# Optimization experiments

Measured on AMD Instinct MI355X. Metric: run time of the kernel, lower is better.

## Reference

```python
import jax, jax.numpy as jnp
import numpy as np

ALPHA = 0.2  # leaky relu slope
NEG = -1e9


def setup_inputs() -> dict:
    key = jax.random.key(0)
    ks = jax.random.split(key, 8)
    B, N, F_IN, H, HID, OUT = 2, 4096, 512, 4, 128, 64
    x = jax.random.normal(ks[0], (B, N, F_IN), dtype=jnp.float32)
    adj = jax.random.randint(ks[1], (B, N, N), 0, 2, dtype=jnp.int32)
    s_in = float(np.sqrt(2.0 / (F_IN + HID)))
    W_heads = jax.random.normal(ks[2], (H, HID, F_IN), dtype=jnp.float32) * s_in
    a1_heads = jax.random.normal(ks[3], (H, HID), dtype=jnp.float32) * 0.1
    a2_heads = jax.random.normal(ks[4], (H, HID), dtype=jnp.float32) * 0.1
    s_out = float(np.sqrt(2.0 / (H * HID + OUT)))
    W_out = jax.random.normal(ks[5], (OUT, H * HID), dtype=jnp.float32) * s_out
    a1_out = jax.random.normal(ks[6], (OUT,), dtype=jnp.float32) * 0.1
    a2_out = jax.random.normal(ks[7], (OUT,), dtype=jnp.float32) * 0.1
    return {"x": x, "adj": adj, "W_heads": W_heads, "a1_heads": a1_heads,
            "a2_heads": a2_heads, "W_out": W_out, "a1_out": a1_out, "a2_out": a2_out}


def _gat_layer(x, adj, W, a1, a2, concat):
    # x: [B,N,F], W: [O,F], a1/a2: [O]
    h = jnp.einsum('bnf,of->bno', x, W)            # [B,N,O]
    f1 = jnp.einsum('bno,o->bn', h, a1)            # [B,N]
    f2 = jnp.einsum('bno,o->bn', h, a2)            # [B,N]
    e = f1[:, :, None] + f2[:, None, :]            # [B,N,N] additive scores
    e = jnp.where(e > 0, e, ALPHA * e)             # leaky relu
    e = jnp.where(adj == 0, NEG, e)                # adjacency mask
    att = jax.nn.softmax(e, axis=2)
    h_prime = jnp.einsum('bnm,bmo->bno', att, h)
    return jax.nn.elu(h_prime) if concat else h_prime


def reference(x, adj, W_heads, a1_heads, a2_heads, W_out, a1_out, a2_out):
    H = W_heads.shape[0]
    heads = [_gat_layer(x, adj, W_heads[i], a1_heads[i], a2_heads[i], True)
             for i in range(H)]
    x_cat = jnp.concatenate(heads, axis=2)         # [B,N,H*HID]
    return _gat_layer(x_cat, adj, W_out, a1_out, a2_out, False)
```

## Files before the change

kernel.cpp:

```cpp
#include <hip/hip_runtime.h>

#define TB 2
#define TN 4096
#define TH 4
#define THID 128
#define TOUT 64
#define NW 128

using f4    = __attribute__((ext_vector_type(4))) float;
using s16x8 = __attribute__((ext_vector_type(8))) short;
using s16x4 = __attribute__((ext_vector_type(4))) short;
using u32x4 = __attribute__((ext_vector_type(4))) unsigned;

static __device__ __forceinline__ short f2bf(float f){
  unsigned u = __float_as_uint(f);
  unsigned r = u + 0x7FFFu + ((u >> 16) & 1u);
  return (short)(r >> 16);
}
static __device__ __forceinline__ float bf2f(short s){
  return __uint_as_float(((unsigned)(unsigned short)s) << 16);
}
static __device__ __forceinline__ unsigned encf(float f){
  unsigned u = __float_as_uint(f);
  return (u & 0x80000000u) ? ~u : (u | 0x80000000u);
}
static __device__ __forceinline__ float decf(unsigned u){
  unsigned v = (u & 0x80000000u) ? (u & 0x7FFFFFFFu) : ~u;
  return __uint_as_float(v);
}
static __device__ __forceinline__ void gll16(const void* g, void* l){
  __builtin_amdgcn_global_load_lds((const __attribute__((address_space(1))) unsigned int*)g,
                                   (__attribute__((address_space(3))) unsigned int*)l, 16, 0, 0);
}
static __device__ __forceinline__ f4 mfma_bf16(s16x8 a, s16x8 b, f4 c){
  return __builtin_amdgcn_mfma_f32_16x16x32_bf16(a, b, c, 0, 0, 0);
}

__global__ void k_pack(const int* __restrict__ adj, unsigned* __restrict__ adjT,
                       unsigned* __restrict__ mx){
  if (blockIdx.x == 0 && threadIdx.x < 16) mx[threadIdx.x] = 0;
  int t = blockIdx.x * 256 + threadIdx.x;
  int n = t & 4095, w = (t >> 12) & 127, b = t >> 19;
  const int4* p = (const int4*)(adj + ((size_t)(b*TN + n))*TN + w*32);
  unsigned m = 0;
#pragma unroll
  for (int i = 0; i < 8; ++i){
    int4 v = p[i];
    m |= (v.x != 0 ? 1u : 0u) << (i*4+0);
    m |= (v.y != 0 ? 1u : 0u) << (i*4+1);
    m |= (v.z != 0 ? 1u : 0u) << (i*4+2);
    m |= (v.w != 0 ? 1u : 0u) << (i*4+3);
  }
  adjT[((size_t)(b*NW + w))*TN + n] = m;
}

__global__ void k_split(const float* __restrict__ x, short* __restrict__ hi, short* __restrict__ lo){
  int t = blockIdx.x * 256 + threadIdx.x;
  f4 v = ((const f4*)x)[t];
  s16x4 h, l;
#pragma unroll
  for (int e = 0; e < 4; ++e){
    short hb = f2bf(v[e]);
    h[e] = hb;
    l[e] = f2bf(v[e] - bf2f(hb));
  }
  ((s16x4*)hi)[t] = h;
  ((s16x4*)lo)[t] = l;
}
__global__ void k_cvt(const float* __restrict__ x, short* __restrict__ o){
  int t = blockIdx.x * 256 + threadIdx.x;
  f4 v = ((const f4*)x)[t];
  s16x4 h;
#pragma unroll
  for (int e = 0; e < 4; ++e) h[e] = f2bf(v[e]);
  ((s16x4*)o)[t] = h;
}

__global__ __launch_bounds__(512, 2) void k_gemm1(
    const short* __restrict__ xh, const short* __restrict__ xl,
    const short* __restrict__ wh, const short* __restrict__ wl,
    const float* __restrict__ a1h, const float* __restrict__ a2h,
    short* __restrict__ hTb, float* __restrict__ f1g,
    float* __restrict__ Qa, float* __restrict__ Sa, unsigned* __restrict__ mx){
  __shared__ short tiles[2][4][8192];
  __shared__ float red[2][128][2];
  __shared__ float bmx[2];
  int tid = threadIdx.x, lane = tid & 63, w = tid >> 6;
  int kgrp = lane >> 4, li = lane & 15;
  int nblk = blockIdx.x >> 6, mblk = blockIdx.x & 63;
  int n0 = nblk * 128, m0 = mblk * 128;
  int wn = w >> 2, wm = w & 3;
  const f4 fz = {0.f, 0.f, 0.f, 0.f};
  f4 acc[4][2];
#pragma unroll
  for (int i = 0; i < 4; ++i)
#pragma unroll
    for (int j = 0; j < 2; ++j) acc[i][j] = fz;

#pragma unroll
  for (int tno = 0; tno < 4; ++tno){
    const short* gb = (tno==0 ? wh : tno==1 ? wl : tno==2 ? xh : xl);
    int r0 = (tno < 2) ? n0 : m0;
#pragma unroll
    for (int i = 0; i < 2; ++i){
      int s = (i*8 + w)*64 + lane;
      int row = s >> 3, c = s & 7, cs = c ^ (row & 7);
      gll16(gb + (size_t)(r0 + row)*512 + cs*8, (char*)tiles[0][tno] + (i*8+w)*1024);
    }
  }
  asm volatile("s_waitcnt vmcnt(0)" ::: "memory");
  __syncthreads();

  for (int kt = 0; kt < 8; ++kt){
    int cur = kt & 1;
    if (kt < 7){
      int k0 = (kt+1) * 64;
#pragma unroll
      for (int tno = 0; tno < 4; ++tno){
        const short* gb = (tno==0 ? wh : tno==1 ? wl : tno==2 ? xh : xl);
        int r0 = (tno < 2) ? n0 : m0;
#pragma unroll
        for (int i = 0; i < 2; ++i){
          int s = (i*8 + w)*64 + lane;
          int row = s >> 3, c = s & 7, cs = c ^ (row & 7);
          gll16(gb + (size_t)(r0 + row)*512 + k0 + cs*8, (char*)tiles[cur^1][tno] + (i*8+w)*1024);
        }
      }
    }
    const char* t0 = (const char*)tiles[cur][0];
    const char* t1 = (const char*)tiles[cur][1];
    const char* t2 = (const char*)tiles[cur][2];
    const char* t3 = (const char*)tiles[cur][3];
#pragma unroll
    for (int ks = 0; ks < 2; ++ks){
      int ck = ks*4 + kgrp;
      s16x8 ah[4], al[4], bh[2], bl[2];
#pragma unroll
      for (int fn = 0; fn < 4; ++fn){
        int row = wn*64 + fn*16 + li;
        int off = row*128 + ((ck ^ (row & 7)) << 4);
        ah[fn] = *(const s16x8*)(t0 + off);
        al[fn] = *(const s16x8*)(t1 + off);
      }
#pragma unroll
      for (int fm = 0; fm < 2; ++fm){
        int row = wm*32 + fm*16 + li;
        int off = row*128 + ((ck ^ (row & 7)) << 4);
        bh[fm] = *(const s16x8*)(t2 + off);
        bl[fm] = *(const s16x8*)(t3 + off);
      }
#pragma unroll
      for (int fn = 0; fn < 4; ++fn)
#pragma unroll
        for (int fm = 0; fm < 2; ++fm)
          acc[fn][fm] = mfma_bf16(ah[fn], bh[fm], acc[fn][fm]);
#pragma unroll
      for (int fn = 0; fn < 4; ++fn)
#pragma unroll
        for (int fm = 0; fm < 2; ++fm)
          acc[fn][fm] = mfma_bf16(ah[fn], bl[fm], acc[fn][fm]);
#pragma unroll
      for (int fn = 0; fn < 4; ++fn)
#pragma unroll
        for (int fm = 0; fm < 2; ++fm)
          acc[fn][fm] = mfma_bf16(al[fn], bh[fm], acc[fn][fm]);
    }
    asm volatile("s_waitcnt vmcnt(0)" ::: "memory");
    __syncthreads();
  }
  int head = nblk;
#pragma unroll
  for (int fn = 0; fn < 4; ++fn){
#pragma unroll
    for (int fm = 0; fm < 2; ++fm){
#pragma unroll
      for (int r = 0; r < 4; ++r){
        int nout = n0 + wn*64 + fn*16 + kgrp*4 + r;
        int m = m0 + wm*32 + fm*16 + li;
        int b = m >> 12, n = m & 4095;
        int hid = nout & 127;
        size_t idx = ((size_t)((b*TH + head)*THID + hid))*TN + n;
        hTb[idx] = f2bf(acc[fn][fm][r]);
      }
    }
  }
  const float* a1p = a1h + head*THID;
  const float* a2p = a2h + head*THID;
  float s1[2] = {0.f, 0.f}, s2[2] = {0.f, 0.f};
#pragma unroll
  for (int fn = 0; fn < 4; ++fn)
#pragma unroll
    for (int r = 0; r < 4; ++r){
      int row = wn*64 + fn*16 + kgrp*4 + r;
      float w1 = a1p[row], w2 = a2p[row];
#pragma unroll
      for (int fm = 0; fm < 2; ++fm){
        s1[fm] = fmaf(acc[fn][fm][r], w1, s1[fm]);
        s2[fm] = fmaf(acc[fn][fm][r], w2, s2[fm]);
      }
    }
#pragma unroll
  for (int fm = 0; fm < 2; ++fm){
    s1[fm] += __shfl_xor(s1[fm], 16); s1[fm] += __shfl_xor(s1[fm], 32);
    s2[fm] += __shfl_xor(s2[fm], 16); s2[fm] += __shfl_xor(s2[fm], 32);
  }
  if (kgrp == 0){
#pragma unroll
    for (int fm = 0; fm < 2; ++fm){
      int col = wm*32 + fm*16 + li;
      red[wn][col][0] = s1[fm];
      red[wn][col][1] = s2[fm];
    }
  }
  __syncthreads();
  if (tid < 128){
    float f1v = red[0][tid][0] + red[1][tid][0];
    float f2v = red[0][tid][1] + red[1][tid][1];
    int m = m0 + tid, b = m >> 12, n = m & 4095;
    int idx = (b*TH + head)*TN + n;
    f1g[idx] = f1v;
    Qa[idx] = expf(f2v);
    Sa[idx] = expf(0.2f*f2v);
    float wmx = f2v;
#pragma unroll
    for (int d = 1; d < 64; d <<= 1) wmx = fmaxf(wmx, __shfl_xor(wmx, d));
    if ((tid & 63) == 0) bmx[tid >> 6] = wmx;
  }
  __syncthreads();
  if (tid == 0){
    int b = m0 >> 12;
    atomicMax(&mx[b*TH + head], encf(fmaxf(bmx[0], bmx[1])));
  }
}

__global__ __launch_bounds__(256, 2) void k_attn1(
    const short* __restrict__ hTb, const float* __restrict__ f1,
    const float* __restrict__ Qa, const float* __restrict__ Sa,
    const unsigned* __restrict__ adjT, const unsigned* __restrict__ mx,
    short* __restrict__ part, float* __restrict__ sums){
  __shared__ short tile[4][8192];
  __shared__ float Qs[1024], Ss[1024];
  __shared__ unsigned abuf[4][256];
  int tid = threadIdx.x, lane = tid & 63, w = tid >> 6;
  int kgrp = lane >> 4, li = lane & 15;
  int bid = blockIdx.x;
  int js = bid >> 8, b = (bid >> 7) & 1, h = (bid >> 5) & 3, rblk = bid & 31;
  int bh = b*TH + h;
  int jbase = js * 1024;
  int r0b = rblk * 128;
  const short* hbase = hTb + ((size_t)bh*THID)*TN;
  const float* Qrow = Qa + (size_t)bh*TN + jbase;
  const float* Srow = Sa + (size_t)bh*TN + jbase;

  auto STAGE = [&](int t){
    int jg = jbase + t*64;
    char* dst = (char*)tile[t & 3];
#pragma unroll
    for (int i = 0; i < 4; ++i){
      int s = (i*4 + w)*64 + lane;
      int row = s >> 3, c = s & 7, cs = c ^ (row & 7);
      gll16(hbase + (size_t)row*TN + jg + cs*8, dst + (i*4+w)*1024);
    }
    int w0 = jg >> 5;
    gll16(adjT + (size_t)(b*NW + w0 + (lane>>5))*TN + r0b + (lane&31)*4, (char*)abuf[t & 3]);
  };

  gll16(Qrow + w*256 + lane*4, (char*)Qs + w*1024);
  gll16(Srow + w*256 + lane*4, (char*)Ss + w*1024);
  STAGE(0); STAGE(1); STAGE(2);

  int r0 = r0b + w*32;
  float Pv[2], Rv[2];
  int lrow[2];
  float mf = decf(mx[bh]);
#pragma unroll
  for (int rf = 0; rf < 2; ++rf){
    int row = r0 + rf*16 + li;
    lrow[rf] = w*32 + rf*16 + li;
    float f1v = f1[bh*TN + row];
    float e = f1v + mf;
    float m = e > 0.f ? e : 0.2f*e;
    Pv[rf] = expf(f1v - m);
    Rv[rf] = expf(0.2f*f1v - m);
  }
  const f4 fz = {0.f,0.f,0.f,0.f};
  f4 acc[2][8];
#pragma unroll
  for (int i = 0; i < 2; ++i)
#pragma unroll
    for (int j = 0; j < 8; ++j) acc[i][j] = fz;
  f4 accs[2] = {fz, fz};
  s16x8 ones;
#pragma unroll
  for (int e = 0; e < 8; ++e) ones[e] = (short)0x3F80;

  for (int jt = 0; jt < 16; ++jt){
    if (jt < 14)       asm volatile("s_waitcnt vmcnt(10)" ::: "memory");
    else if (jt == 14) asm volatile("s_waitcnt vmcnt(5)" ::: "memory");
    else               asm volatile("s_waitcnt vmcnt(0)" ::: "memory");
    __builtin_amdgcn_s_barrier();
    __builtin_amdgcn_sched_barrier(0);
    if (jt < 13) STAGE(jt + 3);

    int j0 = jt*64;
    const char* tp = (const char*)tile[jt & 3];
    const unsigned* ab = abuf[jt & 3];
    unsigned aw0[2], aw1[2];
#pragma unroll
    for (int rf = 0; rf < 2; ++rf){
      aw0[rf] = ab[lrow[rf]];
      aw1[rf] = ab[128 + lrow[rf]];
    }
#pragma unroll
    for (int ks = 0; ks < 2; ++ks){
      int jloc = j0 + ks*32 + kgrp*8;
      float qv[8], sv[8];
      *(f4*)&qv[0] = *(const f4*)&Qs[jloc];
      *(f4*)&qv[4] = *(const f4*)&Qs[jloc+4];
      *(f4*)&sv[0] = *(const f4*)&Ss[jloc];
      *(f4*)&sv[4] = *(const f4*)&Ss[jloc+4];
      s16x8 af[2];
#pragma unroll
      for (int rf = 0; rf < 2; ++rf){
        unsigned word = ks ? aw1[rf] : aw0[rf];
        unsigned byt = (word >> (kgrp*8)) & 0xFFu;
        float P = Pv[rf], R = Rv[rf];
        u32x4 pw;
#pragma unroll
        for (int pe = 0; pe < 4; ++pe){
          float va = fmaxf(P*qv[2*pe],   R*sv[2*pe]);
          float vb = fmaxf(P*qv[2*pe+1], R*sv[2*pe+1]);
          va = (byt & (1u << (2*pe)))   ? va : 0.f;
          vb = (byt & (1u << (2*pe+1))) ? vb : 0.f;
          unsigned ua = __float_as_uint(va) + 0x8000u;
          unsigned ub = __float_as_uint(vb) + 0x8000u;
          pw[pe] = __builtin_amdgcn_perm(ub, ua, 0x07060302);
        }
        af[rf] = __builtin_bit_cast(s16x8, pw);
      }
      accs[0] = mfma_bf16(af[0], ones, accs[0]);
      accs[1] = mfma_bf16(af[1], ones, accs[1]);
#pragma unroll
      for (int cf = 0; cf < 8; ++cf){
        int col = cf*16 + li;
        int off = col*128 + (((ks*4 + kgrp) ^ (col & 7)) << 4);
        s16x8 bfr = *(const s16x8*)(tp + off);
        acc[0][cf] = mfma_bf16(af[0], bfr, acc[0][cf]);
        acc[1][cf] = mfma_bf16(af[1], bfr, acc[1][cf]);
      }
    }
  }
  int sl = js*8 + bh;
  if (li == 0){
#pragma unroll
    for (int rf = 0; rf < 2; ++rf)
#pragma unroll
      for (int r = 0; r < 4; ++r)
        sums[(size_t)sl*TN + r0 + rf*16 + kgrp*4 + r] = accs[rf][r];
  }
#pragma unroll
  for (int rf = 0; rf < 2; ++rf)
#pragma unroll
    for (int cf = 0; cf < 8; ++cf)
#pragma unroll
      for (int r = 0; r < 4; ++r){
        int row = r0 + rf*16 + kgrp*4 + r;
        int hid = cf*16 + li;
        part[((size_t)sl*TN + row)*THID + hid] = f2bf(acc[rf][cf][r]);
      }
}

__global__ void k_comb1(const short* __restrict__ part, const float* __restrict__ sums,
                        short* __restrict__ xcat){
  int t = blockIdx.x*256 + threadIdx.x;
  int hid8 = t & 15, n = (t >> 4) & 4095, h = (t >> 16) & 3, b = t >> 18;
  int bh = b*TH + h;
  float a[8] = {0,0,0,0,0,0,0,0};
  float s = 0.f;
#pragma unroll
  for (int js = 0; js < 4; ++js){
    size_t rowoff = (size_t)(js*8 + bh)*TN + n;
    s16x8 pv = *(const s16x8*)(part + rowoff*THID + hid8*8);
#pragma unroll
    for (int e = 0; e < 8; ++e) a[e] += bf2f(pv[e]);
    s += sums[rowoff];
  }
  float inv = 1.f / s;
  s16x8 o;
#pragma unroll
  for (int e = 0; e < 8; ++e){
    float x = a[e] * inv;
    o[e] = f2bf(x > 0.f ? x : expm1f(x));
  }
  *(s16x8*)(xcat + ((size_t)(b*TN + n))*512 + h*128 + hid8*8) = o;
}

__global__ __launch_bounds__(128) void k_gemm2(
    const short* __restrict__ xcat, const short* __restrict__ wo,
    const float* __restrict__ a1o, const float* __restrict__ a2o,
    short* __restrict__ h2T, float* __restrict__ f1o,
    float* __restrict__ Q2, float* __restrict__ S2, unsigned* __restrict__ mx2){
  int tid = threadIdx.x, lane = tid & 63, w = tid >> 6;
  int kgrp = lane >> 4, li = lane & 15;
  int m0 = blockIdx.x * 32;
  const f4 fz = {0.f,0.f,0.f,0.f};
  f4 acc[4] = {fz, fz, fz, fz};
  int rowA = m0 + w*16 + li;
  for (int kt = 0; kt < 16; ++kt){
    int k = kt*32 + kgrp*8;
    s16x8 a = *(const s16x8*)(xcat + (size_t)rowA*512 + k);
#pragma unroll
    for (int cf = 0; cf < 4; ++cf){
      int col = cf*16 + li;
      s16x8 bfr = *(const s16x8*)(wo + (size_t)col*512 + k);
      acc[cf] = mfma_bf16(a, bfr, acc[cf]);
    }
  }
  float p1[4] = {0,0,0,0}, p2[4] = {0,0,0,0};
#pragma unroll
  for (int cf = 0; cf < 4; ++cf){
    int o = cf*16 + li;
    float w1 = a1o[o], w2 = a2o[o];
#pragma unroll
    for (int r = 0; r < 4; ++r){
      p1[r] = fmaf(acc[cf][r], w1, p1[r]);
      p2[r] = fmaf(acc[cf][r], w2, p2[r]);
    }
  }
#pragma unroll
  for (int r = 0; r < 4; ++r){
#pragma unroll
    for (int d = 1; d < 16; d <<= 1){
      p1[r] += __shfl_xor(p1[r], d);
      p2[r] += __shfl_xor(p2[r], d);
    }
  }
#pragma unroll
  for (int cf = 0; cf < 4; ++cf)
#pragma unroll
    for (int r = 0; r < 4; ++r){
      int row = m0 + w*16 + kgrp*4 + r;
      int o = cf*16 + li;
      int b = row >> 12, n = row & 4095;
      h2T[((size_t)(b*TOUT + o))*TN + n] = f2bf(acc[cf][r]);
    }
  if (li == 0){
#pragma unroll
    for (int r = 0; r < 4; ++r){
      int row = m0 + w*16 + kgrp*4 + r;
      f1o[row] = p1[r];
      Q2[row] = expf(p2[r]);
      S2[row] = expf(0.2f*p2[r]);
    }
  }
  float m2 = fmaxf(fmaxf(p2[0], p2[1]), fmaxf(p2[2], p2[3]));
  m2 = fmaxf(m2, __shfl_xor(m2, 16));
  m2 = fmaxf(m2, __shfl_xor(m2, 32));
  __shared__ float bm[2];
  if (lane == 0) bm[w] = m2;
  __syncthreads();
  if (tid == 0) atomicMax(&mx2[m0 >> 12], encf(fmaxf(bm[0], bm[1])));
}

__global__ __launch_bounds__(256, 3) void k_attn2(
    const short* __restrict__ h2T, const float* __restrict__ f1o,
    const float* __restrict__ Q2, const float* __restrict__ S2,
    const unsigned* __restrict__ adjT, const unsigned* __restrict__ mx2,
    float* __restrict__ part, float* __restrict__ sums){
  __shared__ short tile[4][4096];
  __shared__ float Qs[1024], Ss[1024];
  __shared__ unsigned abuf[4][128];
  int tid = threadIdx.x, lane = tid & 63, w = tid >> 6;
  int kgrp = lane >> 4, li = lane & 15;
  int bid = blockIdx.x;
  int js = bid >> 7, b = (bid >> 6) & 1, rblk = bid & 63;
  int jbase = js * 1024;
  int r0b = rblk * 64;
  const short* hbase = h2T + (size_t)b*TOUT*TN;
  const float* Qrow = Q2 + (size_t)b*TN + jbase;
  const float* Srow = S2 + (size_t)b*TN + jbase;

  auto STAGE = [&](int t){
    int jg = jbase + t*64;
    char* dst = (char*)tile[t & 3];
#pragma unroll
    for (int i = 0; i < 2; ++i){
      int s = (i*4 + w)*64 + lane;
      int row = s >> 3, c = s & 7, cs = c ^ (row & 7);
      gll16(hbase + (size_t)row*TN + jg + cs*8, dst + (i*4+w)*1024);
    }
    int w0 = jg >> 5;
    if (lane < 32)
      gll16(adjT + (size_t)(b*NW + w0 + (lane>>4))*TN + r0b + (lane&15)*4, (char*)abuf[t & 3]);
  };

  gll16(Qrow + w*256 + lane*4, (char*)Qs + w*1024);
  gll16(Srow + w*256 + lane*4, (char*)Ss + w*1024);
  STAGE(0); STAGE(1); STAGE(2);

  int r0 = r0b + w*16;
  int lrow = w*16 + li;
  float mf = decf(mx2[b]);
  float f1v = f1o[b*TN + r0 + li];
  float e0 = f1v + mf;
  float m0v = e0 > 0.f ? e0 : 0.2f*e0;
  float Pv = expf(f1v - m0v);
  float Rv = expf(0.2f*f1v - m0v);
  const f4 fz = {0.f,0.f,0.f,0.f};
  f4 acc[4] = {fz, fz, fz, fz};
  f4 accs = fz;
  s16x8 ones;
#pragma unroll
  for (int e = 0; e < 8; ++e) ones[e] = (short)0x3F80;

  for (int jt = 0; jt < 16; ++jt){
    if (jt < 14)       asm volatile("s_waitcnt vmcnt(6)" ::: "memory");
    else if (jt == 14) asm volatile("s_waitcnt vmcnt(3)" ::: "memory");
    else               asm volatile("s_waitcnt vmcnt(0)" ::: "memory");
    __builtin_amdgcn_s_barrier();
    __builtin_amdgcn_sched_barrier(0);
    if (jt < 13) STAGE(jt + 3);

    int j0 = jt*64;
    const char* tp = (const char*)tile[jt & 3];
    const unsigned* ab = abuf[jt & 3];
    unsigned aw0 = ab[lrow], aw1 = ab[64 + lrow];
#pragma unroll
    for (int ks = 0; ks < 2; ++ks){
      int jloc = j0 + ks*32 + kgrp*8;
      float qv[8], sv[8];
      *(f4*)&qv[0] = *(const f4*)&Qs[jloc];
      *(f4*)&qv[4] = *(const f4*)&Qs[jloc+4];
      *(f4*)&sv[0] = *(const f4*)&Ss[jloc];
      *(f4*)&sv[4] = *(const f4*)&Ss[jloc+4];
      unsigned word = ks ? aw1 : aw0;
      unsigned byt = (word >> (kgrp*8)) & 0xFFu;
      u32x4 pw;
#pragma unroll
      for (int pe = 0; pe < 4; ++pe){
        float va = fmaxf(Pv*qv[2*pe],   Rv*sv[2*pe]);
        float vb = fmaxf(Pv*qv[2*pe+1], Rv*sv[2*pe+1]);
        va = (byt & (1u << (2*pe)))   ? va : 0.f;
        vb = (byt & (1u << (2*pe+1))) ? vb : 0.f;
        unsigned ua = __float_as_uint(va) + 0x8000u;
        unsigned ub = __float_as_uint(vb) + 0x8000u;
        pw[pe] = __builtin_amdgcn_perm(ub, ua, 0x07060302);
      }
      s16x8 af = __builtin_bit_cast(s16x8, pw);
      accs = mfma_bf16(af, ones, accs);
#pragma unroll
      for (int cf = 0; cf < 4; ++cf){
        int col = cf*16 + li;
        int off = col*128 + (((ks*4 + kgrp) ^ (col & 7)) << 4);
        s16x8 bfr = *(const s16x8*)(tp + off);
        acc[cf] = mfma_bf16(af, bfr, acc[cf]);
      }
    }
  }
  int sl = js*2 + b;
  if (li == 0){
#pragma unroll
    for (int r = 0; r < 4; ++r)
      sums[(size_t)sl*TN + r0 + kgrp*4 + r] = accs[r];
  }
#pragma unroll
  for (int cf = 0; cf < 4; ++cf)
#pragma unroll
    for (int r = 0; r < 4; ++r){
      int row = r0 + kgrp*4 + r;
      int o = cf*16 + li;
      part[((size_t)sl*TN + row)*TOUT + o] = acc[cf][r];
    }
}

__global__ void k_comb2(const float* __restrict__ part, const float* __restrict__ sums,
                        float* __restrict__ out){
  int t = blockIdx.x*256 + threadIdx.x;
  int o4 = t & 15, n = (t >> 4) & 4095, b = t >> 16;
  f4 a = {0.f,0.f,0.f,0.f};
  float s = 0.f;
#pragma unroll
  for (int js = 0; js < 4; ++js){
    int sl = js*2 + b;
    a += ((const f4*)part)[((size_t)sl*TN + n)*16 + o4];
    s += sums[(size_t)sl*TN + n];
  }
  f4 r = a / s;
  ((f4*)out)[((size_t)(b*TN + n))*16 + o4] = r;
}

extern "C" void kernel_launch(void* const* d_in, const int* in_sizes, int n_in,
                              void* d_out, int out_size, void* d_ws, size_t ws_size,
                              hipStream_t stream) {
  (void)in_sizes; (void)n_in; (void)out_size; (void)ws_size;
  const float* x       = (const float*)d_in[0];
  const int*   adj     = (const int*)d_in[1];
  const float* W_heads = (const float*)d_in[2];
  const float* a1h     = (const float*)d_in[3];
  const float* a2h     = (const float*)d_in[4];
  const float* W_out   = (const float*)d_in[5];
  const float* a1o     = (const float*)d_in[6];
  const float* a2o     = (const float*)d_in[7];

  char* p = (char*)d_ws;
  auto alloc = [&](size_t sz){ char* r = p; p += (sz + 255) & ~(size_t)255; return r; };
  unsigned* adjT  = (unsigned*) alloc(4ull*1048576);
  short*    wo    = (short*)    alloc(2ull*32768);
  short*    hTb   = (short*)    alloc(2ull*4194304);
  float*    f1    = (float*)    alloc(4ull*32768);
  float*    Qa    = (float*)    alloc(4ull*32768);
  float*    Sa    = (float*)    alloc(4ull*32768);
  unsigned* mx    = (unsigned*) alloc(4ull*16);
  short*    xcat  = (short*)    alloc(2ull*4194304);
  float*    f1o   = (float*)    alloc(4ull*8192);
  float*    Q2    = (float*)    alloc(4ull*8192);
  float*    S2    = (float*)    alloc(4ull*8192);
  short*    h2T   = (short*)    alloc(2ull*524288);
  float*    sums1 = (float*)    alloc(4ull*131072);
  float*    sums2 = (float*)    alloc(4ull*65536);
  char* A = alloc(33554432ull);
  short* xh   = (short*)A;
  short* xl   = (short*)(A + 8388608);
  short* part1 = (short*)A;
  char* Bu = alloc(16777216ull);
  short* wh = (short*)Bu;
  short* wl = (short*)(Bu + 524288);
  float* part2 = (float*)Bu;

  k_pack <<<4096, 256, 0, stream>>>(adj, adjT, mx);
  k_split<<<4096, 256, 0, stream>>>(x, xh, xl);
  k_split<<<256, 256, 0, stream>>>(W_heads, wh, wl);
  k_cvt  <<<32, 256, 0, stream>>>(W_out, wo);
  k_gemm1<<<256, 512, 0, stream>>>(xh, xl, wh, wl, a1h, a2h, hTb, f1, Qa, Sa, mx);
  k_attn1<<<1024, 256, 0, stream>>>(hTb, f1, Qa, Sa, adjT, mx, part1, sums1);
  k_comb1<<<2048, 256, 0, stream>>>(part1, sums1, xcat);
  k_gemm2<<<256, 128, 0, stream>>>(xcat, wo, a1o, a2o, h2T, f1o, Q2, S2, mx + 8);
  k_attn2<<<512, 256, 0, stream>>>(h2T, f1o, Q2, S2, adjT, mx + 8, part2, sums2);
  k_comb2<<<512, 256, 0, stream>>>(part2, sums2, (float*)d_out);
}
```

Baseline: 153.6 us.

## Enlarge attention row tiles and re-split key range with triple buffering

In k_attn1 each block now covers 256 rows (four 16-row fragments per wave) instead of 128, so each staged 64-key hidden tile is reused across twice as many rows and the grid is halved. In k_attn2 row tiles double to 128 and the key range is split into eight 512-wide slices instead of four, which keeps the grid size and doubles the partials that k_comb2 reduces. Both kernels move from 4-deep to 3-deep staging buffers and retune the waitcnt thresholds. The cost is far more accumulator registers in attn1 (4x8 fragments), which may cut occupancy, along with a shallower prefetch pipeline.

Measured after the change: 148.0 us. 3.7% less time.

```diff
diff --git a/kernel.cpp b/kernel.cpp
--- a/kernel.cpp
+++ b/kernel.cpp
@@ -238,23 +238,24 @@
     const float* __restrict__ Qa, const float* __restrict__ Sa,
     const unsigned* __restrict__ adjT, const unsigned* __restrict__ mx,
     short* __restrict__ part, float* __restrict__ sums){
-  __shared__ short tile[4][8192];
+  __shared__ short tile[3][8192];
   __shared__ float Qs[1024], Ss[1024];
-  __shared__ unsigned abuf[4][256];
+  __shared__ unsigned abuf[3][512];
   int tid = threadIdx.x, lane = tid & 63, w = tid >> 6;
   int kgrp = lane >> 4, li = lane & 15;
   int bid = blockIdx.x;
-  int js = bid >> 8, b = (bid >> 7) & 1, h = (bid >> 5) & 3, rblk = bid & 31;
+  int js = bid >> 7, b = (bid >> 6) & 1, h = (bid >> 4) & 3, rblk = bid & 15;
   int bh = b*TH + h;
   int jbase = js * 1024;
-  int r0b = rblk * 128;
+  int r0b = rblk * 256;
   const short* hbase = hTb + ((size_t)bh*THID)*TN;
   const float* Qrow = Qa + (size_t)bh*TN + jbase;
   const float* Srow = Sa + (size_t)bh*TN + jbase;
 
   auto STAGE = [&](int t){
     int jg = jbase + t*64;
-    char* dst = (char*)tile[t & 3];
+    int bi = t % 3;
+    char* dst = (char*)tile[bi];
 #pragma unroll
     for (int i = 0; i < 4; ++i){
       int s = (i*4 + w)*64 + lane;
@@ -262,21 +263,23 @@
       gll16(hbase + (size_t)row*TN + jg + cs*8, dst + (i*4+w)*1024);
     }
     int w0 = jg >> 5;
-    gll16(adjT + (size_t)(b*NW + w0 + (lane>>5))*TN + r0b + (lane&31)*4, (char*)abuf[t & 3]);
+#pragma unroll
+    for (int k = 0; k < 2; ++k)
+      gll16(adjT + (size_t)(b*NW + w0 + k)*TN + r0b + lane*4, (char*)abuf[bi] + k*1024);
   };
 
   gll16(Qrow + w*256 + lane*4, (char*)Qs + w*1024);
   gll16(Srow + w*256 + lane*4, (char*)Ss + w*1024);
-  STAGE(0); STAGE(1); STAGE(2);
-
-  int r0 = r0b + w*32;
-  float Pv[2], Rv[2];
-  int lrow[2];
+  STAGE(0); STAGE(1);
+
+  int r0 = r0b + w*64;
+  float Pv[4], Rv[4];
+  int lrow[4];
   float mf = decf(mx[bh]);
 #pragma unroll
-  for (int rf = 0; rf < 2; ++rf){
+  for (int rf = 0; rf < 4; ++rf){
     int row = r0 + rf*16 + li;
-    lrow[rf] = w*32 + rf*16 + li;
+    lrow[rf] = w*64 + rf*16 + li;
     float f1v = f1[bh*TN + row];
     float e = f1v + mf;
     float m = e > 0.f ? e : 0.2f*e;
@@ -284,32 +287,32 @@
     Rv[rf] = expf(0.2f*f1v - m);
   }
   const f4 fz = {0.f,0.f,0.f,0.f};
-  f4 acc[2][8];
-#pragma unroll
-  for (int i = 0; i < 2; ++i)
+  f4 acc[4][8];
+#pragma unroll
+  for (int i = 0; i < 4; ++i)
 #pragma unroll
     for (int j = 0; j < 8; ++j) acc[i][j] = fz;
-  f4 accs[2] = {fz, fz};
+  f4 accs[4] = {fz, fz, fz, fz};
   s16x8 ones;
 #pragma unroll
   for (int e = 0; e < 8; ++e) ones[e] = (short)0x3F80;
 
   for (int jt = 0; jt < 16; ++jt){
-    if (jt < 14)       asm volatile("s_waitcnt vmcnt(10)" ::: "memory");
-    else if (jt == 14) asm volatile("s_waitcnt vmcnt(5)" ::: "memory");
-    else               asm volatile("s_waitcnt vmcnt(0)" ::: "memory");
+    if (jt < 15) asm volatile("s_waitcnt vmcnt(6)" ::: "memory");
+    else         asm volatile("s_waitcnt vmcnt(0)" ::: "memory");
     __builtin_amdgcn_s_barrier();
     __builtin_amdgcn_sched_barrier(0);
-    if (jt < 13) STAGE(jt + 3);
+    if (jt < 14) STAGE(jt + 2);
 
     int j0 = jt*64;
-    const char* tp = (const char*)tile[jt & 3];
-    const unsigned* ab = abuf[jt & 3];
-    unsigned aw0[2], aw1[2];
-#pragma unroll
-    for (int rf = 0; rf < 2; ++rf){
+    int bi = jt % 3;
+    const char* tp = (const char*)tile[bi];
+    const unsigned* ab = abuf[bi];
+    unsigned aw0[4], aw1[4];
+#pragma unroll
+    for (int rf = 0; rf < 4; ++rf){
       aw0[rf] = ab[lrow[rf]];
-      aw1[rf] = ab[128 + lrow[rf]];
+      aw1[rf] = ab[256 + lrow[rf]];
     }
 #pragma unroll
     for (int ks = 0; ks < 2; ++ks){
@@ -319,9 +322,9 @@
       *(f4*)&qv[4] = *(const f4*)&Qs[jloc+4];
       *(f4*)&sv[0] = *(const f4*)&Ss[jloc];
       *(f4*)&sv[4] = *(const f4*)&Ss[jloc+4];
-      s16x8 af[2];
-#pragma unroll
-      for (int rf = 0; rf < 2; ++rf){
+      s16x8 af[4];
+#pragma unroll
+      for (int rf = 0; rf < 4; ++rf){
         unsigned word = ks ? aw1[rf] : aw0[rf];
         unsigned byt = (word >> (kgrp*8)) & 0xFFu;
         float P = Pv[rf], R = Rv[rf];
@@ -338,28 +341,30 @@
         }
         af[rf] = __builtin_bit_cast(s16x8, pw);
       }
-      accs[0] = mfma_bf16(af[0], ones, accs[0]);
-      accs[1] = mfma_bf16(af[1], ones, accs[1]);
+#pragma unroll
+      for (int rf = 0; rf < 4; ++rf)
+        accs[rf] = mfma_bf16(af[rf], ones, accs[rf]);
 #pragma unroll
       for (int cf = 0; cf < 8; ++cf){
         int col = cf*16 + li;
         int off = col*128 + (((ks*4 + kgrp) ^ (col & 7)) << 4);
         s16x8 bfr = *(const s16x8*)(tp + off);
-        acc[0][cf] = mfma_bf16(af[0], bfr, acc[0][cf]);
-        acc[1][cf] = mfma_bf16(af[1], bfr, acc[1][cf]);
+#pragma unroll
+        for (int rf = 0; rf < 4; ++rf)
+          acc[rf][cf] = mfma_bf16(af[rf], bfr, acc[rf][cf]);
       }
     }
   }
   int sl = js*8 + bh;
   if (li == 0){
 #pragma unroll
-    for (int rf = 0; rf < 2; ++rf)
+    for (int rf = 0; rf < 4; ++rf)
 #pragma unroll
       for (int r = 0; r < 4; ++r)
         sums[(size_t)sl*TN + r0 + rf*16 + kgrp*4 + r] = accs[rf][r];
   }
 #pragma unroll
-  for (int rf = 0; rf < 2; ++rf)
+  for (int rf = 0; rf < 4; ++rf)
 #pragma unroll
     for (int cf = 0; cf < 8; ++cf)
 #pragma unroll
@@ -462,27 +467,28 @@
   if (tid == 0) atomicMax(&mx2[m0 >> 12], encf(fmaxf(bm[0], bm[1])));
 }
 
-__global__ __launch_bounds__(256, 3) void k_attn2(
+__global__ __launch_bounds__(256, 2) void k_attn2(
     const short* __restrict__ h2T, const float* __restrict__ f1o,
     const float* __restrict__ Q2, const float* __restrict__ S2,
     const unsigned* __restrict__ adjT, const unsigned* __restrict__ mx2,
     float* __restrict__ part, float* __restrict__ sums){
-  __shared__ short tile[4][4096];
-  __shared__ float Qs[1024], Ss[1024];
-  __shared__ unsigned abuf[4][128];
+  __shared__ short tile[3][4096];
+  __shared__ float Qs[512], Ss[512];
+  __shared__ unsigned abuf[3][256];
   int tid = threadIdx.x, lane = tid & 63, w = tid >> 6;
   int kgrp = lane >> 4, li = lane & 15;
   int bid = blockIdx.x;
-  int js = bid >> 7, b = (bid >> 6) & 1, rblk = bid & 63;
-  int jbase = js * 1024;
-  int r0b = rblk * 64;
+  int js = bid >> 6, b = (bid >> 5) & 1, rblk = bid & 31;
+  int jbase = js * 512;
+  int r0b = rblk * 128;
   const short* hbase = h2T + (size_t)b*TOUT*TN;
   const float* Qrow = Q2 + (size_t)b*TN + jbase;
   const float* Srow = S2 + (size_t)b*TN + jbase;
 
   auto STAGE = [&](int t){
     int jg = jbase + t*64;
-    char* dst = (char*)tile[t & 3];
+    int bi = t % 3;
+    char* dst = (char*)tile[bi];
 #pragma unroll
     for (int i = 0; i < 2; ++i){
       int s = (i*4 + w)*64 + lane;
@@ -490,41 +496,55 @@
       gll16(hbase + (size_t)row*TN + jg + cs*8, dst + (i*4+w)*1024);
     }
     int w0 = jg >> 5;
-    if (lane < 32)
-      gll16(adjT + (size_t)(b*NW + w0 + (lane>>4))*TN + r0b + (lane&15)*4, (char*)abuf[t & 3]);
+    gll16(adjT + (size_t)(b*NW + w0 + (lane>>5))*TN + r0b + (lane&31)*4, (char*)abuf[bi]);
   };
 
-  gll16(Qrow + w*256 + lane*4, (char*)Qs + w*1024);
-  gll16(Srow + w*256 + lane*4, (char*)Ss + w*1024);
-  STAGE(0); STAGE(1); STAGE(2);
-
-  int r0 = r0b + w*16;
-  int lrow = w*16 + li;
+  if (w < 2) gll16(Qrow + w*256 + lane*4, (char*)Qs + w*1024);
+  else       gll16(Srow + (w-2)*256 + lane*4, (char*)Ss + (w-2)*1024);
+  STAGE(0); STAGE(1);
+
+  int r0 = r0b + w*32;
+  float Pv[2], Rv[2];
+  int lrow[2];
   float mf = decf(mx2[b]);
-  float f1v = f1o[b*TN + r0 + li];
-  float e0 = f1v + mf;
-  float m0v = e0 > 0.f ? e0 : 0.2f*e0;
-  float Pv = expf(f1v - m0v);
-  float Rv = expf(0.2f*f1v - m0v);
+#pragma unroll
+  for (int rf = 0; rf < 2; ++rf){
+    int row = r0 + rf*16 + li;
+    lrow[rf] = w*32 + rf*16 + li;
+    float f1v = f1o[b*TN + row];
+    float e = f1v + mf;
+    float m = e > 0.f ? e : 0.2f*e;
+    Pv[rf] = expf(f1v - m);
+    Rv[rf] = expf(0.2f*f1v - m);
+  }
   const f4 fz = {0.f,0.f,0.f,0.f};
-  f4 acc[4] = {fz, fz, fz, fz};
-  f4 accs = fz;
+  f4 acc[2][4];
+#pragma unroll
+  for (int i = 0; i < 2; ++i)
+#pragma unroll
+    for (int j = 0; j < 4; ++j) acc[i][j] = fz;
+  f4 accs[2] = {fz, fz};
   s16x8 ones;
 #pragma unroll
   for (int e = 0; e < 8; ++e) ones[e] = (short)0x3F80;
 
-  for (int jt = 0; jt < 16; ++jt){
-    if (jt < 14)       asm volatile("s_waitcnt vmcnt(6)" ::: "memory");
-    else if (jt == 14) asm volatile("s_waitcnt vmcnt(3)" ::: "memory");
-    else               asm volatile("s_waitcnt vmcnt(0)" ::: "memory");
+  for (int jt = 0; jt < 8; ++jt){
+    if (jt < 7) asm volatile("s_waitcnt vmcnt(3)" ::: "memory");
+    else        asm volatile("s_waitcnt vmcnt(0)" ::: "memory");
     __builtin_amdgcn_s_barrier();
     __builtin_amdgcn_sched_barrier(0);
-    if (jt < 13) STAGE(jt + 3);
+    if (jt < 6) STAGE(jt + 2);
 
     int j0 = jt*64;
-    const char* tp = (const char*)tile[jt & 3];
-    const unsigned* ab = abuf[jt & 3];
-    unsigned aw0 = ab[lrow], aw1 = ab[64 + lrow];
+    int bi = jt % 3;
+    const char* tp = (const char*)tile[bi];
+    const unsigned* ab = abuf[bi];
+    unsigned aw0[2], aw1[2];
+#pragma unroll
+    for (int rf = 0; rf < 2; ++rf){
+      aw0[rf] = ab[lrow[rf]];
+      aw1[rf] = ab[128 + lrow[rf]];
+    }
 #pragma unroll
     for (int ks = 0; ks < 2; ++ks){
       int jloc = j0 + ks*32 + kgrp*8;
@@ -533,44 +553,55 @@
       *(f4*)&qv[4] = *(const f4*)&Qs[jloc+4];
       *(f4*)&sv[0] = *(const f4*)&Ss[jloc];
       *(f4*)&sv[4] = *(const f4*)&Ss[jloc+4];
-      unsigned word = ks ? aw1 : aw0;
-      unsigned byt = (word >> (kgrp*8)) & 0xFFu;
-      u32x4 pw;
-#pragma unroll
-      for (int pe = 0; pe < 4; ++pe){
-        float va = fmaxf(Pv*qv[2*pe],   Rv*sv[2*pe]);
-        float vb = fmaxf(Pv*qv[2*pe+1], Rv*sv[2*pe+1]);
-        va = (byt & (1u << (2*pe)))   ? va : 0.f;
-        vb = (byt & (1u << (2*pe+1))) ? vb : 0.f;
-        unsigned ua = __float_as_uint(va) + 0x8000u;
-        unsigned ub = __float_as_uint(vb) + 0x8000u;
-        pw[pe] = __builtin_amdgcn_perm(ub, ua, 0x07060302);
-      }
-      s16x8 af = __builtin_bit_cast(s16x8, pw);
-      accs = mfma_bf16(af, ones, accs);
+      s16x8 af[2];
+#pragma unroll
+      for (int rf = 0; rf < 2; ++rf){
+        unsigned word = ks ? aw1[rf] : aw0[rf];
+        unsigned byt = (word >> (kgrp*8)) & 0xFFu;
+        float P = Pv[rf], R = Rv[rf];
+        u32x4 pw;
+#pragma unroll
+        for (int pe = 0; pe < 4; ++pe){
+          float va = fmaxf(P*qv[2*pe],   R*sv[2*pe]);
+          float vb = fmaxf(P*qv[2*pe+1], R*sv[2*pe+1]);
+          va = (byt & (1u << (2*pe)))   ? va : 0.f;
+          vb = (byt & (1u << (2*pe+1))) ? vb : 0.f;
+          unsigned ua = __float_as_uint(va) + 0x8000u;
+          unsigned ub = __float_as_uint(vb) + 0x8000u;
+          pw[pe] = __builtin_amdgcn_perm(ub, ua, 0x07060302);
+        }
+        af[rf] = __builtin_bit_cast(s16x8, pw);
+      }
+      accs[0] = mfma_bf16(af[0], ones, accs[0]);
+      accs[1] = mfma_bf16(af[1], ones, accs[1]);
 #pragma unroll
       for (int cf = 0; cf < 4; ++cf){
         int col = cf*16 + li;
         int off = col*128 + (((ks*4 + kgrp) ^ (col & 7)) << 4);
         s16x8 bfr = *(const s16x8*)(tp + off);
-        acc[cf] = mfma_bf16(af, bfr, acc[cf]);
+        acc[0][cf] = mfma_bf16(af[0], bfr, acc[0][cf]);
+        acc[1][cf] = mfma_bf16(af[1], bfr, acc[1][cf]);
       }
     }
   }
   int sl = js*2 + b;
   if (li == 0){
 #pragma unroll
-    for (int r = 0; r < 4; ++r)
-      sums[(size_t)sl*TN + r0 + kgrp*4 + r] = accs[r];
-  }
-#pragma unroll
-  for (int cf = 0; cf < 4; ++cf)
-#pragma unroll
-    for (int r = 0; r < 4; ++r){
-      int row = r0 + kgrp*4 + r;
-      int o = cf*16 + li;
-      part[((size_t)sl*TN + row)*TOUT + o] = acc[cf][r];
-    }
+    for (int rf = 0; rf < 2; ++rf)
+#pragma unroll
+      for (int r = 0; r < 4; ++r)
+        sums[(size_t)sl*TN + r0 + rf*16 + kgrp*4 + r] = accs[rf][r];
+  }
+#pragma unroll
+  for (int rf = 0; rf < 2; ++rf)
+#pragma unroll
+    for (int cf = 0; cf < 4; ++cf)
+#pragma unroll
+      for (int r = 0; r < 4; ++r){
+        int row = r0 + rf*16 + kgrp*4 + r;
+        int o = cf*16 + li;
+        part[((size_t)sl*TN + row)*TOUT + o] = acc[rf][cf][r];
+      }
 }
 
 __global__ void k_comb2(const float* __restrict__ part, const float* __restrict__ sums,
@@ -580,7 +611,7 @@
   f4 a = {0.f,0.f,0.f,0.f};
   float s = 0.f;
 #pragma unroll
-  for (int js = 0; js < 4; ++js){
+  for (int js = 0; js < 8; ++js){
     int sl = js*2 + b;
     a += ((const f4*)part)[((size_t)sl*TN + n)*16 + o4];
     s += sums[(size_t)sl*TN + n];
@@ -632,7 +663,7 @@
   k_split<<<256, 256, 0, stream>>>(W_heads, wh, wl);
   k_cvt  <<<32, 256, 0, stream>>>(W_out, wo);
   k_gemm1<<<256, 512, 0, stream>>>(xh, xl, wh, wl, a1h, a2h, hTb, f1, Qa, Sa, mx);
-  k_attn1<<<1024, 256, 0, stream>>>(hTb, f1, Qa, Sa, adjT, mx, part1, sums1);
+  k_attn1<<<512, 256, 0, stream>>>(hTb, f1, Qa, Sa, adjT, mx, part1, sums1);
   k_comb1<<<2048, 256, 0, stream>>>(part1, sums1, xcat);
   k_gemm2<<<256, 128, 0, stream>>>(xcat, wo, a1o, a2o, h2T, f1o, Q2, S2, mx + 8);
   k_attn2<<<512, 256, 0, stream>>>(h2T, f1o, Q2, S2, adjT, mx + 8, part2, sums2);
```
